# Kernel tuning notes

Hardware: AMD Instinct MI355X
Metric: run time of the kernel (lower is better)

## Reference

```python
import jax, jax.numpy as jnp
import numpy as np

# Production-scale dims: batch, feature dim, number of hierarchy classes.
B, F, C = 4096, 1024, 2047
DEPTH = 11  # perfect binary tree: levels 0..10, C = 2**11 - 1, parent(i) = (i-1)//2

# Static per-level node index arrays (numpy, so the jitted code sees constants).
LEVELS = [np.arange(2 ** l - 1, 2 ** (l + 1) - 1) for l in range(DEPTH)]


def setup_inputs() -> dict:
    key = jax.random.key(0)
    k1, k2, k3 = jax.random.split(key, 3)
    x = jax.random.normal(k1, (B, F), jnp.float32)
    weight = jax.random.normal(k2, (C, F), jnp.float32) * 0.02  # nn.Linear weight (C, F)
    bias = jnp.zeros((C,), jnp.float32)
    # Original zero-inits pairs; we use small random values so the CRF is non-trivial.
    pairs = jax.random.normal(k3, (C, C, 2, 2), jnp.float32) * 0.1
    return {"x": x, "weight": weight, "bias": bias, "pairs": pairs}


def _crf_marginals(emissions, pairs):
    """Tree-CRF sum-product (forward/backward style) over a binary label tree.

    emissions: (B, C, 2) log-potentials per node per binary label.
    pairs: (C, C, 2, 2); pairs[i, j, yi, yj] is the edge potential for parent i,
    child j (only tree edges are consumed, matching TreeCRFLayer).
    Returns per-node marginal probabilities (B, C, 2).
    """
    alphas = jnp.zeros_like(emissions)
    # Upward messages: leaves -> root, one vectorized step per tree level.
    for l in range(DEPTH - 1, 0, -1):
        idx = LEVELS[l]
        par = (idx - 1) // 2
        local = emissions[:, idx] + alphas[:, idx]                    # (B, n, 2) child label
        pe = pairs[par, idx]                                          # (n, 2, 2) [y_par, y_child]
        msg = jax.nn.logsumexp(pe[None] + local[:, :, None, :], axis=3)  # (B, n, 2)
        alphas = alphas.at[:, par].add(msg)  # siblings share a parent -> scatter-add
    betas = jnp.zeros_like(emissions)
    # Downward messages: root -> leaves.
    for l in range(DEPTH - 1):
        idx = LEVELS[l]
        local = emissions[:, idx] + betas[:, idx]                     # (B, n, 2) parent label
        for ch in (2 * idx + 1, 2 * idx + 2):
            pe = pairs[idx, ch]                                       # (n, 2, 2)
            msg = jax.nn.logsumexp(local[:, :, :, None] + pe[None], axis=2)  # (B, n, 2)
            betas = betas.at[:, ch].set(msg)  # exactly one parent per node
    scores = emissions + alphas + betas
    return jax.nn.softmax(scores, axis=2)  # normalize per node over the 2 labels


def reference(x, weight, bias, pairs):
    e = x @ weight.T + bias                   # (B, C) = Linear(n_features -> n_classes)
    emissions = jnp.stack((-e, e), axis=2)    # (B, C, 2)
    return _crf_marginals(emissions, pairs)[:, :, 1]
```

## Files before the change

kernel.cpp:

```cpp
#include <hip/hip_runtime.h>
#include <math.h>

#define B_DIM 4096
#define F_DIM 1024
#define C_DIM 2047
#define C_PAD 2048
#define DEPTH 11

#define LOG2E 1.4426950408889634f

typedef __attribute__((ext_vector_type(8))) short bf16x8;
typedef __attribute__((ext_vector_type(4))) float f32x4;

#define AS1(p) ((const __attribute__((address_space(1))) void*)(p))
#define AS3(p) ((__attribute__((address_space(3))) void*)(p))

#define XTOT (B_DIM * F_DIM)
#define WTOT (C_PAD * F_DIM)

__device__ __forceinline__ unsigned short f2bf(float f) {
    unsigned int u = __float_as_uint(f);
    unsigned int r = (u + 0x7fffu + ((u >> 16) & 1u)) >> 16;
    return (unsigned short)r;
}
__device__ __forceinline__ float bf2f(unsigned short u) {
    return __uint_as_float(((unsigned int)u) << 16);
}

__global__ __launch_bounds__(256) void cvt_pack_kernel(
    const float* __restrict__ x, const float* __restrict__ w,
    const float* __restrict__ pairs,
    unsigned short* __restrict__ xb, unsigned short* __restrict__ wb,
    float* __restrict__ pk)
{
    const int i = (blockIdx.x * 256 + threadIdx.x) * 4;
    if (i < XTOT) {
        float4 v = *(const float4*)(x + i);
        ushort4 h;
        h.x = f2bf(v.x); h.y = f2bf(v.y); h.z = f2bf(v.z); h.w = f2bf(v.w);
        *(ushort4*)(xb + i) = h;
    } else if (i < XTOT + WTOT) {
        const int j = i - XTOT;
        const int row = j >> 10;
        ushort4 h = {0, 0, 0, 0};
        if (row < C_DIM) {
            float4 v = *(const float4*)(w + j);
            h.x = f2bf(v.x); h.y = f2bf(v.y); h.z = f2bf(v.z); h.w = f2bf(v.w);
        }
        *(ushort4*)(wb + j) = h;
    } else {
        const int c0 = i - XTOT - WTOT;
#pragma unroll
        for (int t = 0; t < 4; ++t) {
            const int c = c0 + t;
            if (c >= 1 && c < C_DIM) {
                const int p = (c - 1) >> 1;
                float4 v = *(const float4*)(pairs + ((size_t)p * C_DIM + c) * 4);
                pk[c + 1]        = v.x * LOG2E;
                pk[c + 1 + 2048] = v.y * LOG2E;
                pk[c + 1 + 4096] = v.z * LOG2E;
                pk[c + 1 + 6144] = v.w * LOG2E;
            }
        }
    }
}

__global__ __launch_bounds__(256) void gemm_bf16_kernel(
    const unsigned short* __restrict__ xb, const unsigned short* __restrict__ wb,
    const float* __restrict__ bias, unsigned short* __restrict__ eb)
{
    __shared__ unsigned short smemA[128 * 32];
    __shared__ unsigned short smemB[128 * 32];

    const int tid  = threadIdx.x;
    const int lane = tid & 63;
    const int wave = tid >> 6;
    const int wr = wave >> 1, wc = wave & 1;

    const int lin = blockIdx.x + blockIdx.y * gridDim.x;
    const int wg  = (lin & 7) * 64 + (lin >> 3);
    const int bn = wg & 15, bm = wg >> 4;

    f32x4 acc[4][4] = {};
    const int r0 = tid >> 2,         c0 = tid & 3;
    const int r1 = (tid + 256) >> 2, c1 = tid & 3;
    const int sc0 = ((c0 ^ ((r0 >> 1) & 3)) << 3);
    const int sc1 = ((c1 ^ ((r1 >> 1) & 3)) << 3);

    const size_t arow0 = (size_t)(bm * 128 + r0) * F_DIM;
    const size_t arow1 = (size_t)(bm * 128 + r1) * F_DIM;
    const size_t brow0 = (size_t)(bn * 128 + r0) * F_DIM;
    const size_t brow1 = (size_t)(bn * 128 + r1) * F_DIM;

    unsigned short* ldsA0 = smemA + wave * 512;
    unsigned short* ldsA1 = smemA + 2048 + wave * 512;
    unsigned short* ldsB0 = smemB + wave * 512;
    unsigned short* ldsB1 = smemB + 2048 + wave * 512;

    const int fra = wr * 64 + (lane & 15);
    const int frb = wc * 64 + (lane & 15);
    const int kc  = lane >> 4;

    for (int k0 = 0; k0 < F_DIM; k0 += 32) {
        __builtin_amdgcn_global_load_lds(AS1(xb + arow0 + k0 + sc0), AS3(ldsA0), 16, 0, 0);
        __builtin_amdgcn_global_load_lds(AS1(xb + arow1 + k0 + sc1), AS3(ldsA1), 16, 0, 0);
        __builtin_amdgcn_global_load_lds(AS1(wb + brow0 + k0 + sc0), AS3(ldsB0), 16, 0, 0);
        __builtin_amdgcn_global_load_lds(AS1(wb + brow1 + k0 + sc1), AS3(ldsB1), 16, 0, 0);
        __syncthreads();

        bf16x8 af[4], bfr[4];
#pragma unroll
        for (int m = 0; m < 4; ++m) {
            const int row = fra + m * 16;
            af[m] = *(const bf16x8*)(smemA + row * 32 + ((kc ^ ((row >> 1) & 3)) << 3));
        }
#pragma unroll
        for (int n = 0; n < 4; ++n) {
            const int row = frb + n * 16;
            bfr[n] = *(const bf16x8*)(smemB + row * 32 + ((kc ^ ((row >> 1) & 3)) << 3));
        }
#pragma unroll
        for (int m = 0; m < 4; ++m)
#pragma unroll
            for (int n = 0; n < 4; ++n)
                acc[m][n] = __builtin_amdgcn_mfma_f32_16x16x32_bf16(
                    af[m], bfr[n], acc[m][n], 0, 0, 0);
        __syncthreads();
    }

    const int colbase = bn * 128 + wc * 64 + (lane & 15);
    const int rowbase = bm * 128 + wr * 64 + ((lane >> 4) << 2);
#pragma unroll
    for (int m = 0; m < 4; ++m)
#pragma unroll
        for (int n = 0; n < 4; ++n) {
            const int gc = colbase + n * 16;
            if (gc < C_DIM) {
                const float bv = bias[gc];
#pragma unroll
                for (int r = 0; r < 4; ++r)
                    eb[(size_t)(rowbase + m * 16 + r) * C_PAD + gc + 1] =
                        f2bf(acc[m][n][r] + bv);
            }
        }
}

#define BMF 64
#define BNF 64
#define BKF 16

__global__ __launch_bounds__(256) void gemm_f32_kernel(
    const float* __restrict__ x, const float* __restrict__ w,
    const float* __restrict__ bias, float* __restrict__ e)
{
    __shared__ float As[BKF][BMF];
    __shared__ float Bs[BKF][BNF];
    const int bn = blockIdx.x, bm = blockIdx.y;
    const int tid = threadIdx.x;
    const int tx = tid & 15, ty = tid >> 4;
    const int m0 = ty * 4, n0 = tx * 4;
    const int lrow = tid >> 2, lc4 = (tid & 3) * 4;
    const int gm = bm * BMF + lrow;
    const int gn = bn * BNF + lrow;
    const bool wvalid = (gn < C_DIM);
    const float* xp = x + (size_t)gm * F_DIM + lc4;
    const float* wp = wvalid ? (w + (size_t)gn * F_DIM + lc4) : w;
    float acc[4][4] = {};
    for (int k0 = 0; k0 < F_DIM; k0 += BKF) {
        float4 av = *(const float4*)(xp + k0);
        float4 bv = make_float4(0.f, 0.f, 0.f, 0.f);
        if (wvalid) bv = *(const float4*)(wp + k0);
        As[lc4 + 0][lrow] = av.x; As[lc4 + 1][lrow] = av.y;
        As[lc4 + 2][lrow] = av.z; As[lc4 + 3][lrow] = av.w;
        Bs[lc4 + 0][lrow] = bv.x; Bs[lc4 + 1][lrow] = bv.y;
        Bs[lc4 + 2][lrow] = bv.z; Bs[lc4 + 3][lrow] = bv.w;
        __syncthreads();
#pragma unroll
        for (int k = 0; k < BKF; ++k) {
            float4 a = *(const float4*)&As[k][m0];
            float4 b = *(const float4*)&Bs[k][n0];
            acc[0][0] += a.x * b.x; acc[0][1] += a.x * b.y; acc[0][2] += a.x * b.z; acc[0][3] += a.x * b.w;
            acc[1][0] += a.y * b.x; acc[1][1] += a.y * b.y; acc[1][2] += a.y * b.z; acc[1][3] += a.y * b.w;
            acc[2][0] += a.z * b.x; acc[2][1] += a.z * b.y; acc[2][2] += a.z * b.z; acc[2][3] += a.z * b.w;
            acc[3][0] += a.w * b.x; acc[3][1] += a.w * b.y; acc[3][2] += a.w * b.z; acc[3][3] += a.w * b.w;
        }
        __syncthreads();
    }
    const int gmo = bm * BMF + m0, gno = bn * BNF + n0;
#pragma unroll
    for (int i = 0; i < 4; ++i)
#pragma unroll
        for (int j = 0; j < 4; ++j) {
            int n = gno + j;
            if (n < C_DIM) e[(size_t)(gmo + i) * C_DIM + n] = acc[i][j] + bias[n];
        }
}

__device__ __forceinline__ float lse2_2(float a, float b) {
    float m = fmaxf(a, b);
    return m + __log2f(1.f + exp2f(fminf(a, b) - m));
}
__device__ __forceinline__ float sigmoid2(float d) {
    return __builtin_amdgcn_rcpf(1.f + exp2f(-d));
}

__global__ __launch_bounds__(256) void crf_wave_kernel(
    const float* __restrict__ pk,
    const unsigned short* __restrict__ eb,
    float* __restrict__ out)
{
    const int lane = threadIdx.x & 63;
    const int wid  = blockIdx.x * 4 + (threadIdx.x >> 6);
    const unsigned short* ebr[2] = {eb + (size_t)(2 * wid) * C_PAD,
                                    eb + (size_t)(2 * wid + 1) * C_PAD};
    float* orow[2] = {out + (size_t)(2 * wid) * C_DIM,
                      out + (size_t)(2 * wid + 1) * C_DIM};
    const float* pkx = pk;
    const float* pky = pk + 2048;
    const float* pkz = pk + 4096;
    const float* pkw = pk + 6144;

    float el[2][4][4], da9[2][4][2];
#pragma unroll
    for (int q = 0; q < 4; ++q) {
        const int bi = 1024 + 4 * lane + 256 * q;
        float4 k4x = *(const float4*)(pkx + bi);
        float4 k4y = *(const float4*)(pky + bi);
        float4 k4z = *(const float4*)(pkz + bi);
        float4 k4w = *(const float4*)(pkw + bi);
        float xr[4] = {k4x.x, k4x.y, k4x.z, k4x.w};
        float yr[4] = {k4y.x, k4y.y, k4y.z, k4y.w};
        float zr[4] = {k4z.x, k4z.y, k4z.z, k4z.w};
        float wr4[4] = {k4w.x, k4w.y, k4w.z, k4w.w};
#pragma unroll
        for (int rr = 0; rr < 2; ++rr) {
            ushort4 ev = *(const ushort4*)(ebr[rr] + bi);
            float er[4] = {bf2f(ev.x) * LOG2E, bf2f(ev.y) * LOG2E,
                           bf2f(ev.z) * LOG2E, bf2f(ev.w) * LOG2E};
            float dm[4];
#pragma unroll
            for (int r = 0; r < 4; ++r) {
                el[rr][q][r] = er[r];
                dm[r] = lse2_2(zr[r] - er[r], wr4[r] + er[r])
                      - lse2_2(xr[r] - er[r], yr[r] + er[r]);
            }
            da9[rr][q][0] = dm[0] + dm[1];
            da9[rr][q][1] = dm[2] + dm[3];
        }
    }

    float e9[2][4][2], da8[2][4];
#pragma unroll
    for (int q = 0; q < 4; ++q) {
        const int bi = 512 + 2 * lane + 128 * q;
        float2 k2x = *(const float2*)(pkx + bi);
        float2 k2y = *(const float2*)(pky + bi);
        float2 k2z = *(const float2*)(pkz + bi);
        float2 k2w = *(const float2*)(pkw + bi);
#pragma unroll
        for (int rr = 0; rr < 2; ++rr) {
            ushort2 ev = *(const ushort2*)(ebr[rr] + bi);
            float e0 = bf2f(ev.x) * LOG2E, e1 = bf2f(ev.y) * LOG2E;
            e9[rr][q][0] = e0; e9[rr][q][1] = e1;
            float dm0 = lse2_2(k2z.x - e0, k2w.x + e0 + da9[rr][q][0])
                      - lse2_2(k2x.x - e0, k2y.x + e0 + da9[rr][q][0]);
            float dm1 = lse2_2(k2z.y - e1, k2w.y + e1 + da9[rr][q][1])
                      - lse2_2(k2x.y - e1, k2y.y + e1 + da9[rr][q][1]);
            da8[rr][q] = dm0 + dm1;
        }
    }

    float e8[2][4], ps8[2][4];
#pragma unroll
    for (int q = 0; q < 4; ++q) {
        const int bi = 256 + lane + 64 * q;
        float kx = pkx[bi], ky = pky[bi], kz = pkz[bi], kw = pkw[bi];
#pragma unroll
        for (int rr = 0; rr < 2; ++rr) {
            float e = bf2f(ebr[rr][bi]) * LOG2E;
            e8[rr][q] = e;
            float dm = lse2_2(kz - e, kw + e + da8[rr][q])
                     - lse2_2(kx - e, ky + e + da8[rr][q]);
            ps8[rr][q] = dm + __shfl_xor(dm, 1, 64);
        }
    }
    float da7[2][2];
    {
        const int s = (2 * lane) & 63;
#pragma unroll
        for (int rr = 0; rr < 2; ++rr) {
            float t00 = __shfl(ps8[rr][0], s, 64), t01 = __shfl(ps8[rr][1], s, 64);
            float t10 = __shfl(ps8[rr][2], s, 64), t11 = __shfl(ps8[rr][3], s, 64);
            da7[rr][0] = (lane >= 32) ? t01 : t00;
            da7[rr][1] = (lane >= 32) ? t11 : t10;
        }
    }

    float e7[2][2], ps7[2][2];
#pragma unroll
    for (int q = 0; q < 2; ++q) {
        const int bi = 128 + lane + 64 * q;
        float kx = pkx[bi], ky = pky[bi], kz = pkz[bi], kw = pkw[bi];
#pragma unroll
        for (int rr = 0; rr < 2; ++rr) {
            float e = bf2f(ebr[rr][bi]) * LOG2E;
            e7[rr][q] = e;
            float dm = lse2_2(kz - e, kw + e + da7[rr][q])
                     - lse2_2(kx - e, ky + e + da7[rr][q]);
            ps7[rr][q] = dm + __shfl_xor(dm, 1, 64);
        }
    }
    float da6[2];
    {
        const int s = (2 * lane) & 63;
#pragma unroll
        for (int rr = 0; rr < 2; ++rr) {
            float t0 = __shfl(ps7[rr][0], s, 64), t1 = __shfl(ps7[rr][1], s, 64);
            da6[rr] = (lane >= 32) ? t1 : t0;
        }
    }

    float e6[2], eup[2][6];
#pragma unroll
    for (int rr = 0; rr < 2; ++rr) {
        e6[rr] = bf2f(ebr[rr][64 + lane]) * LOG2E;
#pragma unroll
        for (int lvl = 0; lvl < 6; ++lvl)
            eup[rr][lvl] = bf2f(ebr[rr][(1 << lvl) + lane]) * LOG2E;
    }

    float daS[2][6];
    {
        float da_cur[2] = {da6[0], da6[1]};
        float e_cur[2]  = {e6[0], e6[1]};
        int cb = 64;
#pragma unroll
        for (int lvl = 5; lvl >= 0; --lvl) {
            const int idx = cb + lane;
            float kx = pkx[idx], ky = pky[idx], kz = pkz[idx], kw = pkw[idx];
#pragma unroll
            for (int rr = 0; rr < 2; ++rr) {
                float m0 = lse2_2(kx - e_cur[rr], ky + e_cur[rr] + da_cur[rr]);
                float m1 = lse2_2(kz - e_cur[rr], kw + e_cur[rr] + da_cur[rr]);
                float dm = m1 - m0;
                float da_new = __shfl(dm, (2 * lane) & 63, 64)
                             + __shfl(dm, (2 * lane + 1) & 63, 64);
                da_cur[rr] = da_new;
                e_cur[rr]  = eup[rr][lvl];
                daS[rr][lvl] = da_new;
            }
            cb = (1 << lvl);
        }
    }

    float db_cur[2] = {0.f, 0.f};
#pragma unroll
    for (int lvl = 0; lvl < 6; ++lvl) {
        const int np = 1 << lvl;
        const int idx = 2 * np + lane;
        float kx = pkx[idx], ky = pky[idx], kz = pkz[idx], kw = pkw[idx];
#pragma unroll
        for (int rr = 0; rr < 2; ++rr) {
            if (lane < np)
                orow[rr][np - 1 + lane] =
                    sigmoid2(2.f * eup[rr][lvl] + daS[rr][lvl] + db_cur[rr]);
            float pdb = __shfl(db_cur[rr], lane >> 1, 64);
            float pe  = __shfl(eup[rr][lvl], lane >> 1, 64);
            db_cur[rr] = lse2_2(-pe + ky, pe + pdb + kw)
                       - lse2_2(-pe + kx, pe + pdb + kz);
        }
    }
    float db6[2] = {db_cur[0], db_cur[1]};
#pragma unroll
    for (int rr = 0; rr < 2; ++rr)
        orow[rr][63 + lane] = sigmoid2(2.f * e6[rr] + da6[rr] + db6[rr]);

    float db7[2][2];
#pragma unroll
    for (int q = 0; q < 2; ++q) {
        const int u = (lane >> 1) + 32 * q;
        const int bi = 128 + lane + 64 * q;
        float kx = pkx[bi], ky = pky[bi], kz = pkz[bi], kw = pkw[bi];
#pragma unroll
        for (int rr = 0; rr < 2; ++rr) {
            float pe  = __shfl(e6[rr], u, 64);
            float pdb = __shfl(db6[rr], u, 64);
            db7[rr][q] = lse2_2(-pe + ky, pe + pdb + kw)
                       - lse2_2(-pe + kx, pe + pdb + kz);
            orow[rr][127 + lane + 64 * q] =
                sigmoid2(2.f * e7[rr][q] + da7[rr][q] + db7[rr][q]);
        }
    }

    float db8[2][4];
#pragma unroll
    for (int q = 0; q < 4; ++q) {
        const int u  = (lane >> 1) + 32 * q;
        const int sl = u & 63;
        const int bi = 256 + lane + 64 * q;
        float kx = pkx[bi], ky = pky[bi], kz = pkz[bi], kw = pkw[bi];
#pragma unroll
        for (int rr = 0; rr < 2; ++rr) {
            float pe  = __shfl(e7[rr][q >> 1], sl, 64);
            float pdb = __shfl(db7[rr][q >> 1], sl, 64);
            db8[rr][q] = lse2_2(-pe + ky, pe + pdb + kw)
                       - lse2_2(-pe + kx, pe + pdb + kz);
            orow[rr][255 + lane + 64 * q] =
                sigmoid2(2.f * e8[rr][q] + da8[rr][q] + db8[rr][q]);
        }
    }

    float db9[2][4][2];
#pragma unroll
    for (int q = 0; q < 4; ++q) {
        const int bi = 512 + 2 * lane + 128 * q;
        float2 k2x = *(const float2*)(pkx + bi);
        float2 k2y = *(const float2*)(pky + bi);
        float2 k2z = *(const float2*)(pkz + bi);
        float2 k2w = *(const float2*)(pkw + bi);
#pragma unroll
        for (int rr = 0; rr < 2; ++rr) {
            const float lp0 = -e8[rr][q], lp1 = e8[rr][q] + db8[rr][q];
            db9[rr][q][0] = lse2_2(lp0 + k2y.x, lp1 + k2w.x)
                          - lse2_2(lp0 + k2x.x, lp1 + k2z.x);
            db9[rr][q][1] = lse2_2(lp0 + k2y.y, lp1 + k2w.y)
                          - lse2_2(lp0 + k2x.y, lp1 + k2z.y);
            orow[rr][511 + 2 * lane + 128 * q] =
                sigmoid2(2.f * e9[rr][q][0] + da9[rr][q][0] + db9[rr][q][0]);
            orow[rr][511 + 2 * lane + 128 * q + 1] =
                sigmoid2(2.f * e9[rr][q][1] + da9[rr][q][1] + db9[rr][q][1]);
        }
    }

#pragma unroll
    for (int q = 0; q < 4; ++q) {
        const int bi = 1024 + 4 * lane + 256 * q;
        float4 k4x = *(const float4*)(pkx + bi);
        float4 k4y = *(const float4*)(pky + bi);
        float4 k4z = *(const float4*)(pkz + bi);
        float4 k4w = *(const float4*)(pkw + bi);
        float xr[4] = {k4x.x, k4x.y, k4x.z, k4x.w};
        float yr[4] = {k4y.x, k4y.y, k4y.z, k4y.w};
        float zr[4] = {k4z.x, k4z.y, k4z.z, k4z.w};
        float wr4[4] = {k4w.x, k4w.y, k4w.z, k4w.w};
#pragma unroll
        for (int rr = 0; rr < 2; ++rr) {
#pragma unroll
            for (int r = 0; r < 4; ++r) {
                const float pe = e9[rr][q][r >> 1], pdb = db9[rr][q][r >> 1];
                float db = lse2_2(-pe + yr[r], pe + pdb + wr4[r])
                         - lse2_2(-pe + xr[r], pe + pdb + zr[r]);
                orow[rr][1023 + 4 * lane + 256 * q + r] =
                    sigmoid2(2.f * el[rr][q][r] + db);
            }
        }
    }
}

__global__ __launch_bounds__(64) void crf_fallback_kernel(
    const float* __restrict__ pairs, float* __restrict__ eo)
{
    __shared__ float se[C_DIM];
    __shared__ float da[1023];
    __shared__ float P0[1024];
    __shared__ float P1[1024];

    const int row  = blockIdx.x;
    const int lane = threadIdx.x;
    float* erow = eo + (size_t)row * C_DIM;

    for (int c = lane; c < C_DIM; c += 64) se[c] = erow[c] * LOG2E;
    __syncthreads();

    float* cur = P0; float* nxt = P1;
    for (int l = DEPTH - 1; l >= 1; --l) {
        const int np = 1 << (l - 1);
        const int pg0 = np - 1;
        const bool leaf = (l == DEPTH - 1);
        for (int i = lane; i < np; i += 64) {
            const int p = pg0 + i;
            float a0 = 0.f, a1 = 0.f;
#pragma unroll
            for (int s = 0; s < 2; ++s) {
                const int c = 2 * p + 1 + s;
                const int jc = 2 * i + s;
                float ca0 = 0.f, ca1 = 0.f;
                if (!leaf) { ca0 = cur[jc * 2]; ca1 = cur[jc * 2 + 1]; }
                const float l0 = -se[c] + ca0;
                const float l1 =  se[c] + ca1;
                float4 pe = *(const float4*)(pairs + ((size_t)p * C_DIM + c) * 4);
                pe.x *= LOG2E; pe.y *= LOG2E; pe.z *= LOG2E; pe.w *= LOG2E;
                a0 += lse2_2(pe.x + l0, pe.y + l1);
                a1 += lse2_2(pe.z + l0, pe.w + l1);
            }
            nxt[i * 2] = a0; nxt[i * 2 + 1] = a1;
            da[p] = a1 - a0;
        }
        __syncthreads();
        float* t = cur; cur = nxt; nxt = t;
    }
    if (lane == 0) erow[0] = sigmoid2(2.f * se[0] + da[0]);

    float* bcur = P0; float* bnxt = P1;
    for (int l = 1; l <= DEPTH - 1; ++l) {
        const int nc = 1 << l;
        const int cg0 = nc - 1;
        const bool top = (l == 1), last = (l == DEPTH - 1);
        for (int j = lane; j < nc; j += 64) {
            const int c = cg0 + j;
            const int p = (c - 1) >> 1;
            const int ip = j >> 1;
            float b0 = 0.f, b1 = 0.f;
            if (!top) { b0 = bcur[ip * 2]; b1 = bcur[ip * 2 + 1]; }
            const float lp0 = -se[p] + b0;
            const float lp1 =  se[p] + b1;
            float4 pe = *(const float4*)(pairs + ((size_t)p * C_DIM + c) * 4);
            pe.x *= LOG2E; pe.y *= LOG2E; pe.z *= LOG2E; pe.w *= LOG2E;
            const float bc0 = lse2_2(lp0 + pe.x, lp1 + pe.z);
            const float bc1 = lse2_2(lp0 + pe.y, lp1 + pe.w);
            if (!last) { bnxt[j * 2] = bc0; bnxt[j * 2 + 1] = bc1; }
            float d = 2.f * se[c] + (bc1 - bc0);
            if (c < 1023) d += da[c];
            erow[c] = sigmoid2(d);
        }
        __syncthreads();
        float* t = bcur; bcur = bnxt; bnxt = t;
    }
}

extern "C" void kernel_launch(void* const* d_in, const int* in_sizes, int n_in,
                              void* d_out, int out_size, void* d_ws, size_t ws_size,
                              hipStream_t stream) {
    const float* x     = (const float*)d_in[0];
    const float* w     = (const float*)d_in[1];
    const float* bias  = (const float*)d_in[2];
    const float* pairs = (const float*)d_in[3];
    float* out = (float*)d_out;

    unsigned short* xb = (unsigned short*)d_ws;
    unsigned short* wb = xb + (size_t)XTOT;
    float* pkbuf = (float*)(wb + (size_t)WTOT);
    unsigned short* ebuf = (unsigned short*)(pkbuf + 4 * 2048);

    const size_t need = (size_t)(XTOT + WTOT) * 2 + (size_t)4 * 2048 * 4
                      + ((size_t)B_DIM * C_PAD + C_PAD) * 2;

    if (ws_size >= need) {
        cvt_pack_kernel<<<(XTOT + WTOT + 2048) / (256 * 4), 256, 0, stream>>>(
            x, w, pairs, xb, wb, pkbuf);
        dim3 ggrid(C_PAD / 128, B_DIM / 128);
        gemm_bf16_kernel<<<ggrid, 256, 0, stream>>>(xb, wb, bias, ebuf);
        crf_wave_kernel<<<B_DIM / 8, 256, 0, stream>>>(pkbuf, ebuf, out);
    } else {
        dim3 ggrid((C_DIM + BNF - 1) / BNF, B_DIM / BMF);
        gemm_f32_kernel<<<ggrid, 256, 0, stream>>>(x, w, bias, out);
        crf_fallback_kernel<<<B_DIM, 64, 0, stream>>>(pairs, out);
    }
}
```

Baseline: 65.37 us.

## Double-buffer GEMM LDS tiles with K=64 stages to overlap loads and MFMA

Reworks the bf16 GEMM main loop so each tile is staged in two LDS buffers, each covering K=64 as two 32-wide slices. The next tile is prefetched with global_load_lds while MFMAs run on the current tile. This halves the number of barriers and hides global-load latency behind compute. LDS use grows from 16KB to 64KB per block, which may reduce occupancy. Correctness also depends on the global_load_lds writes being complete before the single barrier at the end of each iteration.

Result: faster. 63.72 us (-2.5%).

```diff
diff --git a/kernel.cpp b/kernel.cpp
--- a/kernel.cpp
+++ b/kernel.cpp
@@ -69,8 +69,7 @@
     const unsigned short* __restrict__ xb, const unsigned short* __restrict__ wb,
     const float* __restrict__ bias, unsigned short* __restrict__ eb)
 {
-    __shared__ unsigned short smemA[128 * 32];
-    __shared__ unsigned short smemB[128 * 32];
+    __shared__ unsigned short smem[2][2][2][4096];
 
     const int tid  = threadIdx.x;
     const int lane = tid & 63;
@@ -82,51 +81,74 @@
     const int bn = wg & 15, bm = wg >> 4;
 
     f32x4 acc[4][4] = {};
-    const int r0 = tid >> 2,         c0 = tid & 3;
-    const int r1 = (tid + 256) >> 2, c1 = tid & 3;
+
+    const int r0 = tid >> 2,       c0 = tid & 3;
+    const int r1 = 64 + (tid >> 2);
     const int sc0 = ((c0 ^ ((r0 >> 1) & 3)) << 3);
-    const int sc1 = ((c1 ^ ((r1 >> 1) & 3)) << 3);
+    const int sc1 = ((c0 ^ ((r1 >> 1) & 3)) << 3);
 
     const size_t arow0 = (size_t)(bm * 128 + r0) * F_DIM;
     const size_t arow1 = (size_t)(bm * 128 + r1) * F_DIM;
     const size_t brow0 = (size_t)(bn * 128 + r0) * F_DIM;
     const size_t brow1 = (size_t)(bn * 128 + r1) * F_DIM;
 
-    unsigned short* ldsA0 = smemA + wave * 512;
-    unsigned short* ldsA1 = smemA + 2048 + wave * 512;
-    unsigned short* ldsB0 = smemB + wave * 512;
-    unsigned short* ldsB1 = smemB + 2048 + wave * 512;
+    const int lb0 = wave * 512;
+    const int lb1 = 2048 + wave * 512;
 
     const int fra = wr * 64 + (lane & 15);
     const int frb = wc * 64 + (lane & 15);
     const int kc  = lane >> 4;
 
-    for (int k0 = 0; k0 < F_DIM; k0 += 32) {
-        __builtin_amdgcn_global_load_lds(AS1(xb + arow0 + k0 + sc0), AS3(ldsA0), 16, 0, 0);
-        __builtin_amdgcn_global_load_lds(AS1(xb + arow1 + k0 + sc1), AS3(ldsA1), 16, 0, 0);
-        __builtin_amdgcn_global_load_lds(AS1(wb + brow0 + k0 + sc0), AS3(ldsB0), 16, 0, 0);
-        __builtin_amdgcn_global_load_lds(AS1(wb + brow1 + k0 + sc1), AS3(ldsB1), 16, 0, 0);
+#define STAGE(buf, kt)                                                          \
+    {                                                                           \
+        const int kbase = (kt) * 64;                                            \
+        _Pragma("unroll")                                                       \
+        for (int ks = 0; ks < 2; ++ks) {                                        \
+            const int k0 = kbase + ks * 32;                                     \
+            __builtin_amdgcn_global_load_lds(AS1(xb + arow0 + k0 + sc0),        \
+                AS3(&smem[buf][0][ks][lb0]), 16, 0, 0);                         \
+            __builtin_amdgcn_global_load_lds(AS1(xb + arow1 + k0 + sc1),        \
+                AS3(&smem[buf][0][ks][lb1]), 16, 0, 0);                         \
+            __builtin_amdgcn_global_load_lds(AS1(wb + brow0 + k0 + sc0),        \
+                AS3(&smem[buf][1][ks][lb0]), 16, 0, 0);                         \
+            __builtin_amdgcn_global_load_lds(AS1(wb + brow1 + k0 + sc1),        \
+                AS3(&smem[buf][1][ks][lb1]), 16, 0, 0);                         \
+        }                                                                       \
+    }
+
+    const int NT = F_DIM / 64;
+    STAGE(0, 0);
+    __syncthreads();
+
+    for (int kt = 0; kt < NT; ++kt) {
+        const int cur = kt & 1;
+        if (kt + 1 < NT) STAGE(cur ^ 1, kt + 1);
+
+#pragma unroll
+        for (int ks = 0; ks < 2; ++ks) {
+            bf16x8 af[4], bfr[4];
+#pragma unroll
+            for (int m = 0; m < 4; ++m) {
+                const int row = fra + m * 16;
+                af[m] = *(const bf16x8*)(&smem[cur][0][ks]
+                        [row * 32 + ((kc ^ ((row >> 1) & 3)) << 3)]);
+            }
+#pragma unroll
+            for (int n = 0; n < 4; ++n) {
+                const int row = frb + n * 16;
+                bfr[n] = *(const bf16x8*)(&smem[cur][1][ks]
+                        [row * 32 + ((kc ^ ((row >> 1) & 3)) << 3)]);
+            }
+#pragma unroll
+            for (int m = 0; m < 4; ++m)
+#pragma unroll
+                for (int n = 0; n < 4; ++n)
+                    acc[m][n] = __builtin_amdgcn_mfma_f32_16x16x32_bf16(
+                        af[m], bfr[n], acc[m][n], 0, 0, 0);
+        }
         __syncthreads();
-
-        bf16x8 af[4], bfr[4];
-#pragma unroll
-        for (int m = 0; m < 4; ++m) {
-            const int row = fra + m * 16;
-            af[m] = *(const bf16x8*)(smemA + row * 32 + ((kc ^ ((row >> 1) & 3)) << 3));
-        }
-#pragma unroll
-        for (int n = 0; n < 4; ++n) {
-            const int row = frb + n * 16;
-            bfr[n] = *(const bf16x8*)(smemB + row * 32 + ((kc ^ ((row >> 1) & 3)) << 3));
-        }
-#pragma unroll
-        for (int m = 0; m < 4; ++m)
-#pragma unroll
-            for (int n = 0; n < 4; ++n)
-                acc[m][n] = __builtin_amdgcn_mfma_f32_16x16x32_bf16(
-                    af[m], bfr[n], acc[m][n], 0, 0, 0);
-        __syncthreads();
-    }
+    }
+#undef STAGE
 
     const int colbase = bn * 128 + wc * 64 + (lane & 15);
     const int rowbase = bm * 128 + wr * 64 + ((lane >> 4) << 2);
```
